# Performance work log

Measured on AMD Instinct MI355X. Metric: run time of the kernel, lower is better.

Reference implementation:

```python
import jax, jax.numpy as jnp
import numpy as np

# Hyper-params from init_kwargs
H, DM, DA, DP, M, T = 8, 512, 256, 128, 32, 4096
DK, DAh, DPh = DM // H, DA // H, DP // H   # 64, 32, 16
B, K_STEPS = 8, 2048
S = T + K_STEPS          # length of x = memory + x_pre
EPS = 1e-12

def _l2n(x):
    # F.normalize(p=2, dim=-1)
    return x / jnp.maximum(jnp.linalg.norm(x, axis=-1, keepdims=True), EPS)

def setup_inputs() -> dict:
    key = jax.random.key(0)
    ks = jax.random.split(key, 28)
    n = lambda i, s, sc=0.05: jax.random.normal(ks[i], s, jnp.float32) * sc
    return {
        "memory": jax.random.normal(ks[0], (B, S - 1, DM), jnp.float32),
        "x_pre":  jax.random.normal(ks[1], (B, 1, DM), jnp.float32),
        "aux":    jax.random.normal(ks[2], (B, S, DA), jnp.float32),
        "pos":    jax.random.normal(ks[3], (B, S, DP), jnp.float32),
        "Wq": n(4, (H, DK, DM)), "bq": n(5, (H, DK)),
        "Wk": n(6, (H, DK, DM)), "bk": n(7, (H, DK)),
        "Wv": n(8, (H, DK, DM)), "bv": n(9, (H, DK)),
        "Wqa": n(10, (H, DAh, DA)), "bqa": n(11, (H, DAh)),
        "Wka": n(12, (H, DAh, DA)), "bka": n(13, (H, DAh)),
        "Wqp": n(14, (H, DPh, DP)), "bqp": n(15, (H, DPh)),
        "Wkp": n(16, (H, DPh, DP)), "bkp": n(17, (H, DPh)),
        "W_ih": n(18, (3 * DK, DM)), "W_hh": n(19, (3 * DK, DK)),
        "b_ih": n(20, (3 * DK,)), "b_hh": n(21, (3 * DK,)),
        "WO": n(22, (DM, DM)), "bO": n(23, (DM,)),
        "w": n(24, (1, 1), 1.0), "w_a": n(25, (1, 1), 1.0), "w_p": n(26, (1, 1), 1.0),
        "G": (jax.random.uniform(ks[27], (DK, DK)) < 0.5).astype(jnp.int32),
        "k": K_STEPS,
    }

def _forward(memory, x_pre, aux, pos, Wq, bq, Wk, bk, Wv, bv, Wqa, bqa, Wka, bka,
             Wqp, bqp, Wkp, bkp, W_ih, W_hh, b_ih, b_hh, WO, bO, w, w_a, w_p, G, k):
    b = memory.shape[0]
    x = jnp.concatenate([memory, x_pre], axis=1)           # [B, S, DM]
    s = x.shape[1]
    Wn = k + T - M + 1                                     # attention window length
    g = G.astype(x.dtype)
    mask_h = jnp.tile(g, (1, H))[None]                     # [1, DK, DM] per-head SparseLinear mask

    # per-head Q/K node projections (SparseLinear), L2-normalized
    Q = _l2n(jnp.einsum('bsd,hkd->bhsk', x, Wq * mask_h) + bq[None, :, None, :])
    K = _l2n(jnp.einsum('bsd,hkd->bhsk', x, Wk * mask_h) + bk[None, :, None, :])

    # tn_transform_pre: for each position p, mean over the M-step window of Qv[m].K[p+m]
    Qv = Q[:, :, -M:, :]                                   # [B,H,M,DK]
    D = jnp.einsum('bhmd,bhsd->bhms', Qv, K)               # [B,H,M,S]
    p_idx = jnp.arange(Wn)[None, :] + jnp.arange(M)[:, None]   # [M,Wn]
    band = D[:, :, jnp.arange(M)[:, None], p_idx]          # [B,H,M,Wn] band-diagonal gather
    tn = band.mean(axis=2)                                 # [B,H,Wn]

    # aux / pos similarities: only the last query row survives the slice in the source
    QA = _l2n(jnp.einsum('bsa,hca->bhsc', aux, Wqa) + bqa[None, :, None, :])
    KA = _l2n(jnp.einsum('bsa,hca->bhsc', aux, Wka) + bka[None, :, None, :])
    dot2 = jnp.einsum('bhc,bhsc->bhs', QA[:, :, -1, :], KA[:, :, aux.shape[1] - Wn:, :])
    QP = _l2n(jnp.einsum('bsp,hcp->bhsc', pos, Wqp) + bqp[None, :, None, :])
    KP = _l2n(jnp.einsum('bsp,hcp->bhsc', pos, Wkp) + bkp[None, :, None, :])
    dot3 = jnp.einsum('bhc,bhsc->bhs', QP[:, :, -1, :], KP[:, :, pos.shape[1] - Wn:, :])

    attn = jax.nn.softmax(w[0, 0] * tn + w_a[0, 0] * dot2 + w_p[0, 0] * dot3, axis=-1)  # [B,H,Wn]

    # value projection over the history window, weighted by attn[..., :-1]
    xv = x[:, s - Wn:s - 1, :]                             # [B, Wn-1, DM]
    V = jnp.einsum('bsd,hkd->bhsk', xv, Wv * mask_h) + bv[None, :, None, :]
    hist = jnp.einsum('bhw,bhwd->bhd', attn[:, :, :-1], V) # [B,H,DK]

    # sequential GRU over the recent M-1 steps (shared across heads)
    recent = jnp.swapaxes(x[:, -M:-1, :], 0, 1)            # [M-1, B, DM]
    def cell(hprev, xt):
        gi = xt @ W_ih.T + b_ih
        gh = hprev @ W_hh.T + b_hh
        ir, iz, inn = jnp.split(gi, 3, axis=-1)
        hr, hz, hn = jnp.split(gh, 3, axis=-1)
        r = jax.nn.sigmoid(ir + hr)
        z = jax.nn.sigmoid(iz + hz)
        nst = jnp.tanh(inn + r * hn)
        return (1.0 - z) * nst + z * hprev, None
    res, _ = jax.lax.scan(cell, jnp.zeros((b, DK), x.dtype), recent)  # [B, DK]

    # concat per-head deltas (deta[:, :, 1:] just drops the initial zeros column)
    deta = (hist + attn[:, :, -1:] * res[:, None, :]).reshape(b, H * DK)   # [B, DM]
    mask_o = jnp.tile(g, (H, H))                           # [DM, DM] for W_O
    out = x_pre + (deta @ (WO * mask_o).T + bO)[:, None, :]
    return out

def reference(memory, x_pre, aux, pos, Wq, bq, Wk, bk, Wv, bv, Wqa, bqa, Wka, bka,
              Wqp, bqp, Wkp, bkp, W_ih, W_hh, b_ih, b_hh, WO, bO, w, w_a, w_p, G, k):
    return _forward(memory, x_pre, aux, pos, Wq, bq, Wk, bk, Wv, bv, Wqa, bqa, Wka,
                    bka, Wqp, bqp, Wkp, bkp, W_ih, W_hh, b_ih, b_hh, WO, bO,
                    w, w_a, w_p, G, k)
```

## Files before the change

### kernel.cpp

```cpp
#include <hip/hip_runtime.h>
#include <math.h>

#define BB   8
#define S    6144
#define SM1  6143
#define DM   512
#define H    8
#define DK   64
#define M    32
#define WN   6113
#define DA   256
#define DAh  32
#define DP   128
#define DPh  16
#define EPSN 1e-12f

#define WS_WKT    0
#define WS_WKAT   262144
#define WS_WKPT   327680
#define WS_QHAT   344064
#define WS_QAHAT  475136
#define WS_QPHAT  477184
#define WS_LOGITS 478208
#define WS_XBAR   869440
#define WS_ALAST  902208
#define WS_RES    902272
#define WS_GI     902784
#define WS_WQM    950400
#define WS_XBF    1212544
#define N_LOGITS  391232
#define N_XBAR    32768

typedef __attribute__((ext_vector_type(8))) short short8;
typedef __attribute__((ext_vector_type(4))) float f32x4;

__device__ inline unsigned short f2bf(float f) {
    union { float f; unsigned u; } v; v.f = f;
    unsigned r = v.u + 0x7fffu + ((v.u >> 16) & 1u);
    return (unsigned short)(r >> 16);
}
__device__ inline float bf2f(unsigned short u) {
    union { unsigned u; float f; } v; v.u = ((unsigned)u) << 16; return v.f;
}

union S8U { short8 v; unsigned short e[8]; };

#define PREP_NB  2368
#define GI_NB    248
#define QAQP_NB  64
#define XCAST_NB 12288

__global__ __launch_bounds__(256) void prelude_k(
    const float* __restrict__ Wk, const float* __restrict__ Wka,
    const float* __restrict__ Wkp, const float* __restrict__ Wq,
    const int* __restrict__ G,
    unsigned short* __restrict__ wkb, unsigned short* __restrict__ wkab,
    unsigned short* __restrict__ wkpb, float* __restrict__ wqm,
    const float* __restrict__ memory, const float* __restrict__ x_pre,
    const float* __restrict__ W_ih, const float* __restrict__ b_ih,
    float* __restrict__ gi_all, unsigned short* __restrict__ xbf,
    const float* __restrict__ aux, const float* __restrict__ pos,
    const float* __restrict__ Wqa, const float* __restrict__ bqa,
    const float* __restrict__ Wqp, const float* __restrict__ bqp,
    float* __restrict__ qahat, float* __restrict__ qphat)
{
    int bx = blockIdx.x, tid = threadIdx.x;
    __shared__ float pa[32][8];
    __shared__ float pp[16][16];

    if (bx < PREP_NB) {
        int idx = bx * 256 + tid;
        if (idx < H*DM*DK) {
            int k = idx & 63; int d = (idx >> 6) & 511; int h = idx >> 15;
            float v = Wk[(size_t)(h*DK + k)*DM + d] * (float)G[k*DK + (d & 63)];
            wkb[(size_t)h*DM*DK + (((d >> 3)*DK + k) << 3) + (d & 7)] = f2bf(v);
        }
        int i2 = idx - H*DM*DK;
        if (i2 >= 0 && i2 < H*DA*DAh) {
            int h = i2 >> 13; int r = i2 & 8191;
            int j = r & 7; int f = r >> 3;
            int c = f & 31; int a = (f >> 5)*8 + j;
            wkab[i2] = f2bf(Wka[(size_t)(h*DAh + c)*DA + a]);
        }
        int i3 = idx - H*DM*DK - H*DA*DAh;
        if (i3 >= 0 && i3 < H*DP*DPh) {
            int h = i3 >> 11; int r = i3 & 2047;
            int j = r & 7; int f = r >> 3;
            int c = f & 15; int p = (f >> 4)*8 + j;
            wkpb[i3] = f2bf(Wkp[(size_t)(h*DPh + c)*DP + p]);
        }
        int i4 = idx - H*DM*DK - H*DA*DAh - H*DP*DPh;
        if (i4 >= 0 && i4 < H*DK*DM) {
            int d = i4 & 511; int k = (i4 >> 9) & 63;
            wqm[i4] = Wq[i4] * (float)G[k*DK + (d & 63)];
        }
        return;
    }
    if (bx < PREP_NB + GI_NB) {
        if (tid < 192) {
            int gx = bx - PREP_NB;
            int t = gx >> 3, b = gx & 7, c = tid;
            const float* xr = memory + ((size_t)b*SM1 + (S - M) + t)*DM;
            const float* wr = W_ih + (size_t)c*DM;
            float s = b_ih[c];
            for (int d = 0; d < DM; d += 4) {
                float4 x4 = *(const float4*)(xr + d);
                float4 w4 = *(const float4*)(wr + d);
                s += x4.x*w4.x + x4.y*w4.y + x4.z*w4.z + x4.w*w4.w;
            }
            gi_all[((size_t)t*BB + b)*192 + c] = s;
        }
        return;
    }
    if (bx < PREP_NB + GI_NB + QAQP_NB) {
        int bh = bx - PREP_NB - GI_NB;
        int b = bh >> 3, h = bh & 7;
        {
            int c = tid & 31, ch = tid >> 5;
            const float* ar = aux + ((size_t)b*S + (S-1))*DA + ch*32;
            const float* wv = Wqa + (size_t)(h*DAh + c)*DA + ch*32;
            float s = 0.f;
            #pragma unroll
            for (int a = 0; a < 32; a += 4) {
                float4 a4 = *(const float4*)(ar + a);
                float4 w4 = *(const float4*)(wv + a);
                s += a4.x*w4.x + a4.y*w4.y + a4.z*w4.z + a4.w*w4.w;
            }
            pa[c][ch] = s;
        }
        {
            int c = tid & 15, ch = tid >> 4;
            const float* pr = pos + ((size_t)b*S + (S-1))*DP + ch*8;
            const float* wv = Wqp + (size_t)(h*DPh + c)*DP + ch*8;
            float4 a4 = *(const float4*)(pr);
            float4 w4 = *(const float4*)(wv);
            float4 a5 = *(const float4*)(pr + 4);
            float4 w5 = *(const float4*)(wv + 4);
            pp[c][ch] = a4.x*w4.x + a4.y*w4.y + a4.z*w4.z + a4.w*w4.w
                      + a5.x*w5.x + a5.y*w5.y + a5.z*w5.z + a5.w*w5.w;
        }
        __syncthreads();
        if (tid < 32) {
            float q = bqa[h*DAh + tid];
            #pragma unroll
            for (int ch = 0; ch < 8; ++ch) q += pa[tid][ch];
            float ss = q*q;
            #pragma unroll
            for (int d2 = 1; d2 <= 16; d2 <<= 1) ss += __shfl_xor(ss, d2);
            qahat[(size_t)bh*DAh + tid] = q / fmaxf(sqrtf(ss), EPSN);
        } else if (tid >= 64 && tid < 80) {
            int c = tid - 64;
            float q = bqp[h*DPh + c];
            #pragma unroll
            for (int ch = 0; ch < 16; ++ch) q += pp[c][ch];
            float ss = q*q;
            #pragma unroll
            for (int d2 = 1; d2 <= 8; d2 <<= 1) ss += __shfl_xor(ss, d2);
            qphat[(size_t)bh*DPh + c] = q / fmaxf(sqrtf(ss), EPSN);
        }
        return;
    }
    {
        size_t e = ((size_t)(bx - PREP_NB - GI_NB - QAQP_NB)*256 + tid)*8;
        int b = (int)(e / ((size_t)S*DM));
        size_t r = e - (size_t)b*S*DM;
        int t = (int)(r >> 9);
        int d = (int)(r & 511);
        const float* src = (t < SM1) ? memory + ((size_t)b*SM1 + t)*DM + d
                                     : x_pre + (size_t)b*DM + d;
        float4 v0 = *(const float4*)src, v1 = *(const float4*)(src + 4);
        S8U t8;
        t8.e[0]=f2bf(v0.x); t8.e[1]=f2bf(v0.y); t8.e[2]=f2bf(v0.z); t8.e[3]=f2bf(v0.w);
        t8.e[4]=f2bf(v1.x); t8.e[5]=f2bf(v1.y); t8.e[6]=f2bf(v1.z); t8.e[7]=f2bf(v1.w);
        *(short8*)(xbf + e) = t8.v;
    }
}

__global__ __launch_bounds__(256) void qhat_gru_k(
    const float* __restrict__ memory, const float* __restrict__ x_pre,
    const float* __restrict__ wqm, const float* __restrict__ bq,
    float* __restrict__ qhat,
    const float* __restrict__ gi_all, const float* __restrict__ W_hh,
    const float* __restrict__ b_hh, float* __restrict__ res)
{
    int bx = blockIdx.x;
    int tid = threadIdx.x;
    __shared__ float part[2][4][64];

    if (bx < 1024) {
        int mp = bx & 15;
        int h  = (bx >> 4) & 7;
        int b  = bx >> 7;
        int k = tid & 63, dq = tid >> 6;

        int m0 = mp*2;
        int t0 = S - M + m0, t1 = t0 + 1;
        const float* x0 = ((t0 < SM1) ? memory + ((size_t)b*SM1 + t0)*DM
                                      : x_pre + (size_t)b*DM) + dq*128;
        const float* x1 = ((t1 < SM1) ? memory + ((size_t)b*SM1 + t1)*DM
                                      : x_pre + (size_t)b*DM) + dq*128;
        const float* wr = wqm + (size_t)(h*DK + k)*DM + dq*128;

        float s0 = 0.f, s1 = 0.f;
        #pragma unroll 8
        for (int d = 0; d < 128; d += 4) {
            float4 w4 = *(const float4*)(wr + d);
            float4 a4 = *(const float4*)(x0 + d);
            float4 b4 = *(const float4*)(x1 + d);
            s0 += w4.x*a4.x + w4.y*a4.y + w4.z*a4.z + w4.w*a4.w;
            s1 += w4.x*b4.x + w4.y*b4.y + w4.z*b4.z + w4.w*b4.w;
        }

        part[0][dq][k] = s0;
        part[1][dq][k] = s1;
        __syncthreads();

        if (tid < 128) {
            int mi = tid >> 6;
            int kk = tid & 63;
            float q = part[mi][0][kk] + part[mi][1][kk] + part[mi][2][kk] + part[mi][3][kk]
                    + bq[h*DK + kk];
            float ss = q*q;
            #pragma unroll
            for (int d2 = 1; d2 <= 32; d2 <<= 1) ss += __shfl_xor(ss, d2);
            qhat[((size_t)(b*H + h)*M + (m0 + mi))*DK + kk] = q / fmaxf(sqrtf(ss), EPSN);
        }
        return;
    }

    {
        int bg = bx - 1024;
        int b = bg*4 + (tid >> 6);
        int l = tid & 63;

        float w0[64], w1[64], w2[64];
        {
            const float* r0p = W_hh + (size_t)l*DK;
            const float* r1p = W_hh + (size_t)(64 + l)*DK;
            const float* r2p = W_hh + (size_t)(128 + l)*DK;
            #pragma unroll
            for (int i = 0; i < 16; ++i) {
                float4 a = *(const float4*)(r0p + i*4);
                w0[i*4]=a.x; w0[i*4+1]=a.y; w0[i*4+2]=a.z; w0[i*4+3]=a.w;
                float4 c = *(const float4*)(r1p + i*4);
                w1[i*4]=c.x; w1[i*4+1]=c.y; w1[i*4+2]=c.z; w1[i*4+3]=c.w;
                float4 e = *(const float4*)(r2p + i*4);
                w2[i*4]=e.x; w2[i*4+1]=e.y; w2[i*4+2]=e.z; w2[i*4+3]=e.w;
            }
        }
        float bh0 = b_hh[l], bh1 = b_hh[64 + l], bh2 = b_hh[128 + l];

        float h = 0.f;
        const float* g0 = gi_all + (size_t)b*192;
        float gr = g0[l], gz = g0[64 + l], gn = g0[128 + l];

        #pragma unroll 1
        for (int t = 0; t < 31; ++t) {
            float a0 = bh0, a1 = bh1, a2 = bh2;
            #pragma unroll
            for (int k = 0; k < 64; ++k) {
                float hk = __int_as_float(__builtin_amdgcn_readlane(__float_as_int(h), k));
                a0 += hk * w0[k];
                a1 += hk * w1[k];
                a2 += hk * w2[k];
            }
            float ngr = 0.f, ngz = 0.f, ngn = 0.f;
            if (t < 30) {
                const float* g2 = gi_all + ((size_t)(t+1)*BB + b)*192;
                ngr = g2[l]; ngz = g2[64 + l]; ngn = g2[128 + l];
            }
            float r = 1.f / (1.f + expf(-(gr + a0)));
            float z = 1.f / (1.f + expf(-(gz + a1)));
            float n = tanhf(gn + r * a2);
            h = (1.f - z)*n + z*h;
            gr = ngr; gz = ngz; gn = ngn;
        }
        res[b*DK + l] = h;
    }
}

#define SMEM_BYTES 16640

__device__ __forceinline__ void kproj3_body(int bxx, int tid, unsigned char* smemraw,
    const unsigned short* __restrict__ xbf, const unsigned short* __restrict__ wkb,
    const float* __restrict__ bk, const float* __restrict__ qhat,
    const float* __restrict__ wscal, float* __restrict__ logits)
{
    int tile = bxx % 96, h = (bxx / 96) & 7, b = bxx / (96*8);
    int t0 = tile * 64;
    int wave = tid >> 6, lane = tid & 63;
    int quad = lane >> 4, l16 = lane & 15;

    typedef unsigned short row72[72];
    row72* Qs = (row72*)smemraw;
    row72* Kb = (row72*)(smemraw + 32*72*2);
    float* tnloc = (float*)(smemraw + 96*72*2);

    {
        const float* qsrc = qhat + (size_t)(b*H + h)*M*DK;
        int i = tid * 8;
        float4 a0 = *(const float4*)(qsrc + i);
        float4 a1 = *(const float4*)(qsrc + i + 4);
        S8U t8;
        t8.e[0]=f2bf(a0.x); t8.e[1]=f2bf(a0.y); t8.e[2]=f2bf(a0.z); t8.e[3]=f2bf(a0.w);
        t8.e[4]=f2bf(a1.x); t8.e[5]=f2bf(a1.y); t8.e[6]=f2bf(a1.z); t8.e[7]=f2bf(a1.w);
        *(short8*)&Qs[i >> 6][i & 63] = t8.v;
    }
    if (tid < 95) tnloc[tid] = 0.f;

    f32x4 acc[4];
    #pragma unroll
    for (int nt = 0; nt < 4; ++nt) acc[nt] = (f32x4){0.f,0.f,0.f,0.f};

    const unsigned short* xrow = xbf + ((size_t)b*S + t0 + wave*16 + l16)*DM;
    const unsigned short* wh = wkb + (size_t)h*DM*DK;

    #pragma unroll
    for (int ch = 0; ch < 4; ++ch) {
        #pragma unroll
        for (int ks = 0; ks < 4; ++ks) {
            short8 a = *(const short8*)(xrow + ch*128 + ks*32 + quad*8);
            #pragma unroll
            for (int nt = 0; nt < 4; ++nt) {
                short8 bf = *(const short8*)(wh + (((ch*16 + ks*4 + quad)*DK) + nt*16 + l16)*8);
                acc[nt] = __builtin_amdgcn_mfma_f32_16x16x32_bf16(a, bf, acc[nt], 0, 0, 0);
            }
        }
    }

    {
        float vv[4][4];
        float ss[4] = {0.f, 0.f, 0.f, 0.f};
        #pragma unroll
        for (int nt = 0; nt < 4; ++nt) {
            float bkv = bk[h*DK + nt*16 + l16];
            #pragma unroll
            for (int reg = 0; reg < 4; ++reg) {
                float v = acc[nt][reg] + bkv;
                vv[nt][reg] = v;
                ss[reg] += v*v;
            }
        }
        #pragma unroll
        for (int d2 = 1; d2 <= 8; d2 <<= 1)
            #pragma unroll
            for (int reg = 0; reg < 4; ++reg) ss[reg] += __shfl_xor(ss[reg], d2);
        #pragma unroll
        for (int reg = 0; reg < 4; ++reg) {
            float inv = 1.f / fmaxf(sqrtf(ss[reg]), EPSN);
            #pragma unroll
            for (int nt = 0; nt < 4; ++nt)
                Kb[wave*16 + quad*4 + reg][nt*16 + l16] = f2bf(vv[nt][reg] * inv);
        }
    }
    __syncthreads();

    {
        int mtile = wave & 1;
        int thalf = (wave >> 1) * 32;
        f32x4 acc2[2];
        acc2[0] = (f32x4){0.f,0.f,0.f,0.f};
        acc2[1] = (f32x4){0.f,0.f,0.f,0.f};
        #pragma unroll
        for (int ks = 0; ks < 2; ++ks) {
            short8 a = *(const short8*)&Qs[mtile*16 + l16][ks*32 + quad*8];
            #pragma unroll
            for (int nt = 0; nt < 2; ++nt) {
                short8 kf = *(const short8*)&Kb[thalf + nt*16 + l16][ks*32 + quad*8];
                acc2[nt] = __builtin_amdgcn_mfma_f32_16x16x32_bf16(a, kf, acc2[nt], 0, 0, 0);
            }
        }
        int m0 = mtile*16 + quad*4;
        #pragma unroll
        for (int nt = 0; nt < 2; ++nt) {
            int tl = thalf + nt*16 + l16;
            #pragma unroll
            for (int reg = 0; reg < 4; ++reg) {
                int mm = m0 + reg;
                int j = t0 + tl - mm;
                if (j >= 0 && j < WN)
                    atomicAdd(&tnloc[tl - mm + 31], acc2[nt][reg]);
            }
        }
    }
    __syncthreads();
    if (tid < 95) {
        int j = t0 + tid - 31;
        if (j >= 0 && j < WN)
            atomicAdd(&logits[(size_t)(b*H + h)*WN + j], wscal[0]*(1.f/32.f)*tnloc[tid]);
    }
}

__device__ __forceinline__ void ka_body(int g, int tid, unsigned char* smemraw,
    const float* __restrict__ aux, const unsigned short* __restrict__ wkab,
    const float* __restrict__ bka, const float* __restrict__ qahat,
    const float* __restrict__ wa, float* __restrict__ logits)
{
    int tile = g % 96;
    int hp   = (g / 96) & 3;
    int b    = g / 384;
    int j0   = tile * 64;
    int wave = tid >> 6, lane = tid & 63;
    int quad = lane >> 4, l16 = lane & 15;

    unsigned short* Xa = (unsigned short*)smemraw;

    int r = tid >> 2, seg = tid & 3;
    int jcl = j0 + r; if (jcl > WN-1) jcl = WN-1;
    int tt = r >> 4, lo = r & 15;
    const float* arb = aux + ((size_t)b*S + (31 + jcl))*DA;

    f32x4 acc[2][2];
    #pragma unroll
    for (int hi = 0; hi < 2; ++hi)
        #pragma unroll
        for (int nt = 0; nt < 2; ++nt) acc[hi][nt] = (f32x4){0.f,0.f,0.f,0.f};

    #pragma unroll
    for (int p = 0; p < 2; ++p) {
        if (p) __syncthreads();
        {
            const float* ar = arb + p*128 + seg*32;
            #pragma unroll
            for (int gg = 0; gg < 4; ++gg) {
                float4 v0 = *(const float4*)(ar + gg*8);
                float4 v1 = *(const float4*)(ar + gg*8 + 4);
                S8U t8;
                t8.e[0]=f2bf(v0.x); t8.e[1]=f2bf(v0.y); t8.e[2]=f2bf(v0.z); t8.e[3]=f2bf(v0.w);
                t8.e[4]=f2bf(v1.x); t8.e[5]=f2bf(v1.y); t8.e[6]=f2bf(v1.z); t8.e[7]=f2bf(v1.w);
                *(short8*)&Xa[(tt*4 + seg)*520 + (gg*16 + lo)*8] = t8.v;
            }
        }
        __syncthreads();
        #pragma unroll
        for (int hi = 0; hi < 2; ++hi) {
            int h = hp*2 + hi;
            const unsigned short* wsrc = wkab + (size_t)h*DA*DAh;
            #pragma unroll
            for (int ks = 0; ks < 4; ++ks) {
                short8 a = *(const short8*)&Xa[(wave*4 + ks)*520 + lane*8];
                #pragma unroll
                for (int nt = 0; nt < 2; ++nt) {
                    short8 bf = *(const short8*)(wsrc +
                        (size_t)((((p*4 + ks)*4 + quad)*32) + nt*16 + l16)*8);
                    acc[hi][nt] = __builtin_amdgcn_mfma_f32_16x16x32_bf16(
                        a, bf, acc[hi][nt], 0, 0, 0);
                }
            }
        }
    }

    float wav = wa[0];
    #pragma unroll
    for (int hi = 0; hi < 2; ++hi) {
        int h = hp*2 + hi;
        float bk0 = bka[h*DAh + l16], bk1 = bka[h*DAh + 16 + l16];
        float q0 = qahat[(size_t)(b*H + h)*DAh + l16];
        float q1 = qahat[(size_t)(b*H + h)*DAh + 16 + l16];
        #pragma unroll
        for (int reg = 0; reg < 4; ++reg) {
            float v0 = acc[hi][0][reg] + bk0;
            float v1 = acc[hi][1][reg] + bk1;
            float ss = v0*v0 + v1*v1;
            float dp = v0*q0 + v1*q1;
            #pragma unroll
            for (int d2 = 1; d2 <= 8; d2 <<= 1) {
                ss += __shfl_xor(ss, d2);
                dp += __shfl_xor(dp, d2);
            }
            if (l16 == 0) {
                int j = j0 + wave*16 + quad*4 + reg;
                if (j < WN)
                    atomicAdd(&logits[(size_t)(b*H + h)*WN + j],
                              wav * dp / fmaxf(sqrtf(ss), EPSN));
            }
        }
    }
}

__device__ __forceinline__ void kp_body(int g, int tid, unsigned char* smemraw,
    const float* __restrict__ pos, const unsigned short* __restrict__ wkpb,
    const float* __restrict__ bkp, const float* __restrict__ qphat,
    const float* __restrict__ wp, float* __restrict__ logits)
{
    int tile = g % 96;
    int hp   = (g / 96) & 3;
    int b    = g / 384;
    int j0   = tile * 64;
    int wave = tid >> 6, lane = tid & 63;
    int quad = lane >> 4, l16 = lane & 15;

    unsigned short* Xp = (unsigned short*)smemraw;

    {
        int r = tid >> 2, seg = tid & 3;
        int j = j0 + r; if (j > WN-1) j = WN-1;
        const float* pr = pos + ((size_t)b*S + (31 + j))*DP + seg*32;
        int tt = r >> 4, lo = r & 15;
        #pragma unroll
        for (int gg = 0; gg < 4; ++gg) {
            float4 v0 = *(const float4*)(pr + gg*8);
            float4 v1 = *(const float4*)(pr + gg*8 + 4);
            int d0 = seg*32 + gg*8;
            int ks = d0 >> 5, qd = (d0 >> 3) & 3;
            S8U t8;
            t8.e[0]=f2bf(v0.x); t8.e[1]=f2bf(v0.y); t8.e[2]=f2bf(v0.z); t8.e[3]=f2bf(v0.w);
            t8.e[4]=f2bf(v1.x); t8.e[5]=f2bf(v1.y); t8.e[6]=f2bf(v1.z); t8.e[7]=f2bf(v1.w);
            *(short8*)&Xp[(tt*4 + ks)*520 + (qd*16 + lo)*8] = t8.v;
        }
    }
    __syncthreads();

    float wpv = wp[0];
    #pragma unroll
    for (int hi = 0; hi < 2; ++hi) {
        int h = hp*2 + hi;
        const unsigned short* wsrc = wkpb + (size_t)h*DP*DPh;
        f32x4 acc = (f32x4){0.f,0.f,0.f,0.f};
        #pragma unroll
        for (int ks = 0; ks < 4; ++ks) {
            short8 a = *(const short8*)&Xp[(wave*4 + ks)*520 + lane*8];
            short8 bf = *(const short8*)(wsrc + (size_t)(((ks*4 + quad)*16) + l16)*8);
            acc = __builtin_amdgcn_mfma_f32_16x16x32_bf16(a, bf, acc, 0, 0, 0);
        }
        float bk0 = bkp[h*DPh + l16];
        float q0 = qphat[(size_t)(b*H + h)*DPh + l16];
        #pragma unroll
        for (int reg = 0; reg < 4; ++reg) {
            float v = acc[reg] + bk0;
            float ss = v*v;
            float dp = v*q0;
            #pragma unroll
            for (int d2 = 1; d2 <= 8; d2 <<= 1) {
                ss += __shfl_xor(ss, d2);
                dp += __shfl_xor(dp, d2);
            }
            if (l16 == 0) {
                int j = j0 + wave*16 + quad*4 + reg;
                if (j < WN)
                    atomicAdd(&logits[(size_t)(b*H + h)*WN + j],
                              wpv * dp / fmaxf(sqrtf(ss), EPSN));
            }
        }
    }
}

#define KA_NB 3072
__global__ __launch_bounds__(256, 4) void proj_fused_k(
    const unsigned short* __restrict__ xbf, const unsigned short* __restrict__ wkb,
    const float* __restrict__ bk, const float* __restrict__ qhat,
    const float* __restrict__ w,
    const float* __restrict__ aux, const unsigned short* __restrict__ wkab,
    const float* __restrict__ bka, const float* __restrict__ qahat,
    const float* __restrict__ wa,
    const float* __restrict__ pos, const unsigned short* __restrict__ wkpb,
    const float* __restrict__ bkp, const float* __restrict__ qphat,
    const float* __restrict__ wp,
    float* __restrict__ logits)
{
    __shared__ __align__(16) unsigned char smemraw[SMEM_BYTES];
    int bx = blockIdx.x;
    int g = bx >> 2, r = bx & 3;
    int tid = threadIdx.x;
    if (r < 2)
        kproj3_body(g*2 + r, tid, smemraw, xbf, wkb, bk, qhat, w, logits);
    else if (r == 2)
        ka_body(g, tid, smemraw, aux, wkab, bka, qahat, wa, logits);
    else
        kp_body(g, tid, smemraw, pos, wkpb, bkp, qphat, wp, logits);
}

__global__ __launch_bounds__(256, 2) void ka_only_k(
    const float* __restrict__ aux, const unsigned short* __restrict__ wkab,
    const float* __restrict__ bka, const float* __restrict__ qahat,
    const float* __restrict__ wa, float* __restrict__ logits)
{
    __shared__ __align__(16) unsigned char smemraw[SMEM_BYTES];
    ka_body(blockIdx.x, threadIdx.x, smemraw, aux, wkab, bka, qahat, wa, logits);
}
__global__ __launch_bounds__(256, 2) void kp_only_k(
    const float* __restrict__ pos, const unsigned short* __restrict__ wkpb,
    const float* __restrict__ bkp, const float* __restrict__ qphat,
    const float* __restrict__ wp, float* __restrict__ logits)
{
    __shared__ __align__(16) unsigned char smemraw[SMEM_BYTES];
    kp_body(blockIdx.x, threadIdx.x, smemraw, pos, wkpb, bkp, qphat, wp, logits);
}

__global__ __launch_bounds__(256, 2) void kproj_band_mfma2(
    const float* __restrict__ memory, const float* __restrict__ x_pre,
    const unsigned short* __restrict__ wkb, const float* __restrict__ bk,
    const float* __restrict__ qhat, const float* __restrict__ wscal,
    float* __restrict__ logits)
{
    int bx = blockIdx.x;
    int hp = bx & 3, b = (bx >> 2) & 7, tile = bx >> 5;
    int t0 = tile * 128;
    int tid = threadIdx.x;
    int wave = tid >> 6, lane = tid & 63;
    int quad = lane >> 4, l16 = lane & 15;

    __shared__ unsigned short Xf[32*520];
    __shared__ unsigned short Wf[16*520];
    __shared__ unsigned short Kb[128][72];
    __shared__ unsigned short Qs[M][72];
    __shared__ float tnloc[159];

    if (tid < 159) tnloc[tid] = 0.f;
    {
        int h = hp*2;
        const float* qsrc = qhat + (size_t)(b*H + h)*M*DK;
        int i = tid * 8;
        float4 a0 = *(const float4*)(qsrc + i);
        float4 a1 = *(const float4*)(qsrc + i + 4);
        S8U t8;
        t8.e[0]=f2bf(a0.x); t8.e[1]=f2bf(a0.y); t8.e[2]=f2bf(a0.z); t8.e[3]=f2bf(a0.w);
        t8.e[4]=f2bf(a1.x); t8.e[5]=f2bf(a1.y); t8.e[6]=f2bf(a1.z); t8.e[7]=f2bf(a1.w);
        *(short8*)&Qs[i >> 6][i & 63] = t8.v;
    }

    f32x4 acc[2][2][4];
    #pragma unroll
    for (int hi = 0; hi < 2; ++hi)
        #pragma unroll
        for (int mt = 0; mt < 2; ++mt)
            #pragma unroll
            for (int nt = 0; nt < 4; ++nt) acc[hi][mt][nt] = (f32x4){0.f,0.f,0.f,0.f};

    for (int ch = 0; ch < 4; ++ch) {
        __syncthreads();
        {
            int r = tid >> 1, half = tid & 1;
            int t = t0 + r;
            const float* xr = ((t < SM1) ? (memory + ((size_t)b*SM1 + t)*DM)
                                         : (x_pre + (size_t)b*DM)) + ch*128 + half*64;
            int tt = r >> 4, lo = r & 15;
            #pragma unroll
            for (int g = 0; g < 8; ++g) {
                float4 v0 = *(const float4*)(xr + g*8);
                float4 v1 = *(const float4*)(xr + g*8 + 4);
                int d0 = half*64 + g*8;
                int ks = d0 >> 5, qd = (d0 >> 3) & 3;
                S8U t8;
                t8.e[0]=f2bf(v0.x); t8.e[1]=f2bf(v0.y); t8.e[2]=f2bf(v0.z); t8.e[3]=f2bf(v0.w);
                t8.e[4]=f2bf(v1.x); t8.e[5]=f2bf(v1.y); t8.e[6]=f2bf(v1.z); t8.e[7]=f2bf(v1.w);
                *(short8*)&Xf[(tt*4 + ks)*520 + (qd*16 + lo)*8] = t8.v;
            }
        }
        {
            const unsigned short* src = wkb + (size_t)(hp*2)*DM*DK + (size_t)ch*8192;
            #pragma unroll
            for (int i = 0; i < 4; ++i) {
                int f = tid + 256*i;
                *(short8*)&Wf[(f >> 6)*520 + (f & 63)*8] = *(const short8*)(src + f*8);
            }
        }
        __syncthreads();
        #pragma unroll
        for (int ks = 0; ks < 4; ++ks) {
            short8 a0 = *(const short8*)&Xf[((wave*2 + 0)*4 + ks)*520 + lane*8];
            short8 a1 = *(const short8*)&Xf[((wave*2 + 1)*4 + ks)*520 + lane*8];
            #pragma unroll
            for (int nt = 0; nt < 4; ++nt) {
                short8 bf = *(const short8*)&Wf[(ks*4 + quad)*520 + (nt*16 + l16)*8];
                acc[0][0][nt] = __builtin_amdgcn_mfma_f32_16x16x32_bf16(a0, bf, acc[0][0][nt], 0, 0, 0);
                acc[0][1][nt] = __builtin_amdgcn_mfma_f32_16x16x32_bf16(a1, bf, acc[0][1][nt], 0, 0, 0);
            }
        }
        __syncthreads();
        {
            const unsigned short* src = wkb + (size_t)(hp*2 + 1)*DM*DK + (size_t)ch*8192;
            #pragma unroll
            for (int i = 0; i < 4; ++i) {
                int f = tid + 256*i;
                *(short8*)&Wf[(f >> 6)*520 + (f & 63)*8] = *(const short8*)(src + f*8);
            }
        }
        __syncthreads();
        #pragma unroll
        for (int ks = 0; ks < 4; ++ks) {
            short8 a0 = *(const short8*)&Xf[((wave*2 + 0)*4 + ks)*520 + lane*8];
            short8 a1 = *(const short8*)&Xf[((wave*2 + 1)*4 + ks)*520 + lane*8];
            #pragma unroll
            for (int nt = 0; nt < 4; ++nt) {
                short8 bf = *(const short8*)&Wf[(ks*4 + quad)*520 + (nt*16 + l16)*8];
                acc[1][0][nt] = __builtin_amdgcn_mfma_f32_16x16x32_bf16(a0, bf, acc[1][0][nt], 0, 0, 0);
                acc[1][1][nt] = __builtin_amdgcn_mfma_f32_16x16x32_bf16(a1, bf, acc[1][1][nt], 0, 0, 0);
            }
        }
    }

    float wom = wscal[0] * (1.f/32.f);

    for (int hi = 0; hi < 2; ++hi) {
        int h = hp*2 + hi;
        __syncthreads();
        {
            float ss[2][4];
            float vv[2][4][4];
            #pragma unroll
            for (int mt = 0; mt < 2; ++mt)
                #pragma unroll
                for (int reg = 0; reg < 4; ++reg) ss[mt][reg] = 0.f;
            #pragma unroll
            for (int nt = 0; nt < 4; ++nt) {
                float bkv = bk[h*DK + nt*16 + l16];
                #pragma unroll
                for (int mt = 0; mt < 2; ++mt)
                    #pragma unroll
                    for (int reg = 0; reg < 4; ++reg) {
                        float v = acc[hi][mt][nt][reg] + bkv;
                        vv[mt][nt][reg] = v;
                        ss[mt][reg] += v*v;
                    }
            }
            #pragma unroll
            for (int d2 = 1; d2 <= 8; d2 <<= 1)
                #pragma unroll
                for (int mt = 0; mt < 2; ++mt)
                    #pragma unroll
                    for (int reg = 0; reg < 4; ++reg)
                        ss[mt][reg] += __shfl_xor(ss[mt][reg], d2);
            #pragma unroll
            for (int mt = 0; mt < 2; ++mt) {
                float inv[4];
                #pragma unroll
                for (int reg = 0; reg < 4; ++reg)
                    inv[reg] = 1.f / fmaxf(sqrtf(ss[mt][reg]), EPSN);
                #pragma unroll
                for (int nt = 0; nt < 4; ++nt)
                    #pragma unroll
                    for (int reg = 0; reg < 4; ++reg)
                        Kb[wave*32 + mt*16 + quad*4 + reg][nt*16 + l16] =
                            f2bf(vv[mt][nt][reg] * inv[reg]);
            }
        }
        __syncthreads();
        {
            f32x4 acc2[2][2];
            #pragma unroll
            for (int mt = 0; mt < 2; ++mt)
                #pragma unroll
                for (int nt = 0; nt < 2; ++nt) acc2[mt][nt] = (f32x4){0.f,0.f,0.f,0.f};
            #pragma unroll
            for (int ks = 0; ks < 2; ++ks) {
                short8 qa0 = *(const short8*)&Qs[l16     ][ks*32 + quad*8];
                short8 qa1 = *(const short8*)&Qs[16 + l16][ks*32 + quad*8];
                #pragma unroll
                for (int nt = 0; nt < 2; ++nt) {
                    short8 kf = *(const short8*)&Kb[wave*32 + nt*16 + l16][ks*32 + quad*8];
                    acc2[0][nt] = __builtin_amdgcn_mfma_f32_16x16x32_bf16(qa0, kf, acc2[0][nt], 0, 0, 0);
                    acc2[1][nt] = __builtin_amdgcn_mfma_f32_16x16x32_bf16(qa1, kf, acc2[1][nt], 0, 0, 0);
                }
            }
            #pragma unroll
            for (int mt = 0; mt < 2; ++mt)
                #pragma unroll
                for (int nt = 0; nt < 2; ++nt) {
                    int tcol = wave*32 + nt*16 + l16;
                    #pragma unroll
                    for (int reg = 0; reg < 4; ++reg) {
                        int m = mt*16 + quad*4 + reg;
                        int j = t0 + tcol - m;
                        if (j >= 0 && j < WN)
                            atomicAdd(&tnloc[tcol - m + 31], acc2[mt][nt][reg]);
                    }
                }
        }
        __syncthreads();
        if (tid < 159) {
            int j = t0 + tid - 31;
            if (j >= 0 && j < WN)
                atomicAdd(&logits[(size_t)(b*H + h)*WN + j], wom * tnloc[tid]);
            tnloc[tid] = 0.f;
        }
        if (hi == 0) {
            const float* qsrc = qhat + (size_t)(b*H + h + 1)*M*DK;
            int i = tid * 8;
            float4 a0 = *(const float4*)(qsrc + i);
            float4 a1 = *(const float4*)(qsrc + i + 4);
            S8U t8;
            t8.e[0]=f2bf(a0.x); t8.e[1]=f2bf(a0.y); t8.e[2]=f2bf(a0.z); t8.e[3]=f2bf(a0.w);
            t8.e[4]=f2bf(a1.x); t8.e[5]=f2bf(a1.y); t8.e[6]=f2bf(a1.z); t8.e[7]=f2bf(a1.w);
            *(short8*)&Qs[i >> 6][i & 63] = t8.v;
        }
    }
}

__global__ __launch_bounds__(1024) void softmax_k(float* __restrict__ logits,
                                                  float* __restrict__ alast)
{
    int bh = blockIdx.x;
    float* L = logits + (size_t)bh*WN;
    __shared__ float red[1024];
    int tid = threadIdx.x;
    float mx = -1e30f;
    for (int j = tid; j < WN; j += 1024) mx = fmaxf(mx, L[j]);
    red[tid] = mx; __syncthreads();
    for (int s2 = 512; s2 > 0; s2 >>= 1) {
        if (tid < s2) red[tid] = fmaxf(red[tid], red[tid+s2]);
        __syncthreads();
    }
    mx = red[0]; __syncthreads();
    float sm = 0.f;
    for (int j = tid; j < WN; j += 1024) sm += expf(L[j] - mx);
    red[tid] = sm; __syncthreads();
    for (int s2 = 512; s2 > 0; s2 >>= 1) {
        if (tid < s2) red[tid] += red[tid+s2];
        __syncthreads();
    }
    float inv = 1.f / red[0];
    for (int j = tid; j < WN; j += 1024) {
        float a = expf(L[j] - mx) * inv;
        L[j] = a;
        if (j == WN-1) alast[bh] = a;
    }
}

#define JC2 96
__global__ __launch_bounds__(256) void xbar_bf_k(
    const unsigned short* __restrict__ xbf, const float* __restrict__ attn,
    float* __restrict__ xbar)
{
    int chunk = blockIdx.x & 63;
    int b = blockIdx.x >> 6;
    int j0 = chunk * JC2;
    int lim = (WN-1) - j0; if (lim > JC2) lim = JC2; if (lim < 0) lim = 0;
    __shared__ float al[H][JC2];
    int tid = threadIdx.x;
    for (int i = tid; i < H*JC2; i += 256) {
        int hh = i / JC2, jj = i - hh*JC2;
        al[hh][jj] = (jj < lim) ? attn[(size_t)(b*H + hh)*WN + j0 + jj] : 0.f;
    }
    __syncthreads();
    int d0 = tid * 2;
    const unsigned* p = (const unsigned*)(xbf + ((size_t)b*S + 31 + j0)*DM + d0);
    float acc[H][2];
    #pragma unroll
    for (int hh = 0; hh < H; ++hh) { acc[hh][0] = 0.f; acc[hh][1] = 0.f; }
    #pragma unroll 4
    for (int jj = 0; jj < lim; ++jj) {
        unsigned u = p[(size_t)jj*(DM/2)];
        float x0 = bf2f((unsigned short)(u & 0xffff));
        float x1 = bf2f((unsigned short)(u >> 16));
        #pragma unroll
        for (int hh = 0; hh < H; ++hh) {
            float a = al[hh][jj];
            acc[hh][0] += a * x0;
            acc[hh][1] += a * x1;
        }
    }
    #pragma unroll
    for (int hh = 0; hh < H; ++hh) {
        atomicAdd(&xbar[(size_t)(b*H+hh)*DM + d0],     acc[hh][0]);
        atomicAdd(&xbar[(size_t)(b*H+hh)*DM + d0 + 1], acc[hh][1]);
    }
}

#define JC 191
__global__ __launch_bounds__(256) void xbar_k(
    const float* __restrict__ memory, const float* __restrict__ attn,
    float* __restrict__ xbar)
{
    int chunk = blockIdx.x & 31;
    int b = blockIdx.x >> 5;
    int j0 = chunk * JC;
    __shared__ float al[H][JC];
    int tid = threadIdx.x;
    for (int i = tid; i < H*JC; i += 256) {
        int hh = i / JC, jj = i - hh*JC;
        al[hh][jj] = attn[(size_t)(b*H + hh)*WN + j0 + jj];
    }
    __syncthreads();
    int d0 = tid * 2;
    float acc[H][2];
    #pragma unroll
    for (int hh = 0; hh < H; ++hh) { acc[hh][0] = 0.f; acc[hh][1] = 0.f; }
    for (int jj = 0; jj < JC; ++jj) {
        int t = 31 + j0 + jj;
        const float2 xv = *(const float2*)(memory + ((size_t)b*SM1 + t)*DM + d0);
        #pragma unroll
        for (int hh = 0; hh < H; ++hh) {
            float a = al[hh][jj];
            acc[hh][0] += a * xv.x;
            acc[hh][1] += a * xv.y;
        }
    }
    #pragma unroll
    for (int hh = 0; hh < H; ++hh) {
        atomicAdd(&xbar[(size_t)(b*H+hh)*DM + d0],     acc[hh][0]);
        atomicAdd(&xbar[(size_t)(b*H+hh)*DM + d0 + 1], acc[hh][1]);
    }
}

__global__ __launch_bounds__(512) void final_k(
    const float* __restrict__ x_pre, const float* __restrict__ xbar,
    const float* __restrict__ Wv, const float* __restrict__ bv,
    const float* __restrict__ WO, const float* __restrict__ bO,
    const float* __restrict__ alast, const float* __restrict__ res,
    const int* __restrict__ G, float* __restrict__ out)
{
    int b = blockIdx.x;
    int tid = threadIdx.x;
    __shared__ float gl[64*64];
    __shared__ float deta[512];
    for (int i = tid; i < 4096; i += 512) gl[i] = (float)G[(i & 63)*64 + (i >> 6)];
    __syncthreads();
    int h = tid >> 6, dk = tid & 63;
    float ala = alast[b*H + h];
    const float* xb  = xbar + (size_t)(b*H + h)*DM;
    const float* wvr = Wv + (size_t)tid*DM;
    const float* gcol = gl + dk;
    float s = 0.f;
    for (int e = 0; e < DM; e += 4) {
        float4 wv4 = *(const float4*)(wvr + e);
        float4 xb4 = *(const float4*)(xb + e);
        int eb = e & 63;
        s += wv4.x*gcol[eb*64]     *xb4.x + wv4.y*gcol[(eb+1)*64]*xb4.y
           + wv4.z*gcol[(eb+2)*64]*xb4.z + wv4.w*gcol[(eb+3)*64]*xb4.w;
    }
    float hist = s + bv[tid]*(1.f - ala);
    deta[tid] = hist + ala * res[b*DK + dk];
    __syncthreads();
    int dpos = tid;
    const float* wor = WO + (size_t)dpos*DM;
    const float* gcol2 = gl + (dpos & 63);
    float o = 0.f;
    for (int jj = 0; jj < DM; jj += 4) {
        float4 wo4 = *(const float4*)(wor + jj);
        int jb = jj & 63;
        o += wo4.x*gcol2[jb*64]     *deta[jj]   + wo4.y*gcol2[(jb+1)*64]*deta[jj+1]
           + wo4.z*gcol2[(jb+2)*64]*deta[jj+2] + wo4.w*gcol2[(jb+3)*64]*deta[jj+3];
    }
    out[(size_t)b*DM + dpos] = x_pre[(size_t)b*DM + dpos] + o + bO[dpos];
}

extern "C" void kernel_launch(void* const* d_in, const int* in_sizes, int n_in,
                              void* d_out, int out_size, void* d_ws, size_t ws_size,
                              hipStream_t stream)
{
    const float* memory = (const float*)d_in[0];
    const float* x_pre  = (const float*)d_in[1];
    const float* aux    = (const float*)d_in[2];
    const float* pos    = (const float*)d_in[3];
    const float* Wq  = (const float*)d_in[4];
    const float* bq  = (const float*)d_in[5];
    const float* Wk  = (const float*)d_in[6];
    const float* bk  = (const float*)d_in[7];
    const float* Wv  = (const float*)d_in[8];
    const float* bv  = (const float*)d_in[9];
    const float* Wqa = (const float*)d_in[10];
    const float* bqa = (const float*)d_in[11];
    const float* Wka = (const float*)d_in[12];
    const float* bka = (const float*)d_in[13];
    const float* Wqp = (const float*)d_in[14];
    const float* bqp = (const float*)d_in[15];
    const float* Wkp = (const float*)d_in[16];
    const float* bkp = (const float*)d_in[17];
    const float* W_ih = (const float*)d_in[18];
    const float* W_hh = (const float*)d_in[19];
    const float* b_ih = (const float*)d_in[20];
    const float* b_hh = (const float*)d_in[21];
    const float* WO  = (const float*)d_in[22];
    const float* bO  = (const float*)d_in[23];
    const float* w   = (const float*)d_in[24];
    const float* w_a = (const float*)d_in[25];
    const float* w_p = (const float*)d_in[26];
    const int*   G   = (const int*)d_in[27];
    (void)in_sizes; (void)n_in; (void)out_size;

    float* ws = (float*)d_ws;
    unsigned short* wkb  = (unsigned short*)(ws + WS_WKT);
    unsigned short* wkab = (unsigned short*)(ws + WS_WKAT);
    unsigned short* wkpb = (unsigned short*)(ws + WS_WKPT);
    float* qhat   = ws + WS_QHAT;
    float* qahat  = ws + WS_QAHAT;
    float* qphat  = ws + WS_QPHAT;
    float* logits = ws + WS_LOGITS;
    float* xbar   = ws + WS_XBAR;
    float* alast  = ws + WS_ALAST;
    float* resb   = ws + WS_RES;
    float* gi_all = ws + WS_GI;
    float* wqm    = ws + WS_WQM;
    unsigned short* xbf = (unsigned short*)(ws + WS_XBF);
    float* outp   = (float*)d_out;

    const size_t need = ((size_t)WS_XBF + 12582912) * 4;
    const bool big = (ws_size >= need);

    hipMemsetAsync(logits, 0, (size_t)(N_LOGITS + N_XBAR)*sizeof(float), stream);

    prelude_k<<<big ? (PREP_NB + GI_NB + QAQP_NB + XCAST_NB)
                    : (PREP_NB + GI_NB + QAQP_NB), 256, 0, stream>>>(
        Wk, Wka, Wkp, Wq, G, wkb, wkab, wkpb, wqm,
        memory, x_pre, W_ih, b_ih, gi_all, xbf,
        aux, pos, Wqa, bqa, Wqp, bqp, qahat, qphat);

    qhat_gru_k<<<1026, 256, 0, stream>>>(memory, x_pre, wqm, bq, qhat,
                                         gi_all, W_hh, b_hh, resb);

    if (big) {
        proj_fused_k<<<12288, 256, 0, stream>>>(
            xbf, wkb, bk, qhat, w,
            aux, wkab, bka, qahat, w_a,
            pos, wkpb, bkp, qphat, w_p, logits);
    } else {
        kproj_band_mfma2<<<48*BB*4, 256, 0, stream>>>(memory, x_pre, wkb, bk, qhat,
                                                      w, logits);
        ka_only_k<<<KA_NB, 256, 0, stream>>>(aux, wkab, bka, qahat, w_a, logits);
        kp_only_k<<<KA_NB, 256, 0, stream>>>(pos, wkpb, bkp, qphat, w_p, logits);
    }

    softmax_k<<<BB*H, 1024, 0, stream>>>(logits, alast);

    if (big)
        xbar_bf_k<<<BB*64, 256, 0, stream>>>(xbf, logits, xbar);
    else
        xbar_k<<<BB*32, 256, 0, stream>>>(memory, logits, xbar);

    final_k<<<BB, 512, 0, stream>>>(x_pre, xbar, Wv, bv, WO, bO, alast, resb, G, outp);
}
```

Measured before the change: 607.1 us.

## Process more heads per block in fused projection kernel to reuse input tiles

The key-projection body now computes two heads per block, reusing each loaded bf16 x fragment for both heads' MFMAs. The aux and pos bodies now handle four heads per block instead of two, so each staged input tile serves more heads. The fused grid is halved to match. This cuts redundant global reads of x, aux and pos and the bf16 conversion work, in exchange for more accumulator registers and fewer blocks, which may reduce occupancy or latency hiding.

```diff
diff --git a/kernel.cpp b/kernel.cpp
--- a/kernel.cpp
+++ b/kernel.cpp
@@ -279,115 +279,132 @@
     }
 }
 
-#define SMEM_BYTES 16640
-
-__device__ __forceinline__ void kproj3_body(int bxx, int tid, unsigned char* smemraw,
+#define SMEM_BYTES 18816
+
+__device__ __forceinline__ void kproj2h_body(int bxx, int tid, unsigned char* smemraw,
     const unsigned short* __restrict__ xbf, const unsigned short* __restrict__ wkb,
     const float* __restrict__ bk, const float* __restrict__ qhat,
     const float* __restrict__ wscal, float* __restrict__ logits)
 {
-    int tile = bxx % 96, h = (bxx / 96) & 7, b = bxx / (96*8);
+    int tile = bxx % 96, hp = (bxx / 96) & 3, b = bxx / 384;
+    int h0 = hp*2;
     int t0 = tile * 64;
     int wave = tid >> 6, lane = tid & 63;
     int quad = lane >> 4, l16 = lane & 15;
 
     typedef unsigned short row72[72];
     row72* Qs = (row72*)smemraw;
-    row72* Kb = (row72*)(smemraw + 32*72*2);
-    float* tnloc = (float*)(smemraw + 96*72*2);
+    row72* Kb = (row72*)(smemraw + 64*72*2);
+    float* tnloc = (float*)(smemraw + 128*72*2);
 
     {
-        const float* qsrc = qhat + (size_t)(b*H + h)*M*DK;
         int i = tid * 8;
-        float4 a0 = *(const float4*)(qsrc + i);
-        float4 a1 = *(const float4*)(qsrc + i + 4);
-        S8U t8;
-        t8.e[0]=f2bf(a0.x); t8.e[1]=f2bf(a0.y); t8.e[2]=f2bf(a0.z); t8.e[3]=f2bf(a0.w);
-        t8.e[4]=f2bf(a1.x); t8.e[5]=f2bf(a1.y); t8.e[6]=f2bf(a1.z); t8.e[7]=f2bf(a1.w);
-        *(short8*)&Qs[i >> 6][i & 63] = t8.v;
+        #pragma unroll
+        for (int hi = 0; hi < 2; ++hi) {
+            const float* qsrc = qhat + (size_t)(b*H + h0 + hi)*M*DK;
+            float4 a0 = *(const float4*)(qsrc + i);
+            float4 a1 = *(const float4*)(qsrc + i + 4);
+            S8U t8;
+            t8.e[0]=f2bf(a0.x); t8.e[1]=f2bf(a0.y); t8.e[2]=f2bf(a0.z); t8.e[3]=f2bf(a0.w);
+            t8.e[4]=f2bf(a1.x); t8.e[5]=f2bf(a1.y); t8.e[6]=f2bf(a1.z); t8.e[7]=f2bf(a1.w);
+            *(short8*)&Qs[hi*32 + (i >> 6)][i & 63] = t8.v;
+        }
     }
     if (tid < 95) tnloc[tid] = 0.f;
 
-    f32x4 acc[4];
-    #pragma unroll
-    for (int nt = 0; nt < 4; ++nt) acc[nt] = (f32x4){0.f,0.f,0.f,0.f};
+    f32x4 acc[2][4];
+    #pragma unroll
+    for (int hi = 0; hi < 2; ++hi)
+        #pragma unroll
+        for (int nt = 0; nt < 4; ++nt) acc[hi][nt] = (f32x4){0.f,0.f,0.f,0.f};
 
     const unsigned short* xrow = xbf + ((size_t)b*S + t0 + wave*16 + l16)*DM;
-    const unsigned short* wh = wkb + (size_t)h*DM*DK;
+    const unsigned short* wh0 = wkb + (size_t)h0*DM*DK;
+    const unsigned short* wh1 = wh0 + (size_t)DM*DK;
 
     #pragma unroll
     for (int ch = 0; ch < 4; ++ch) {
         #pragma unroll
         for (int ks = 0; ks < 4; ++ks) {
             short8 a = *(const short8*)(xrow + ch*128 + ks*32 + quad*8);
+            size_t boff = (size_t)(((ch*16 + ks*4 + quad)*DK))*8;
             #pragma unroll
             for (int nt = 0; nt < 4; ++nt) {
-                short8 bf = *(const short8*)(wh + (((ch*16 + ks*4 + quad)*DK) + nt*16 + l16)*8);
-                acc[nt] = __builtin_amdgcn_mfma_f32_16x16x32_bf16(a, bf, acc[nt], 0, 0, 0);
-            }
-        }
-    }
-
-    {
-        float vv[4][4];
-        float ss[4] = {0.f, 0.f, 0.f, 0.f};
-        #pragma unroll
-        for (int nt = 0; nt < 4; ++nt) {
-            float bkv = bk[h*DK + nt*16 + l16];
+                short8 bf0 = *(const short8*)(wh0 + boff + (nt*16 + l16)*8);
+                short8 bf1 = *(const short8*)(wh1 + boff + (nt*16 + l16)*8);
+                acc[0][nt] = __builtin_amdgcn_mfma_f32_16x16x32_bf16(a, bf0, acc[0][nt], 0, 0, 0);
+                acc[1][nt] = __builtin_amdgcn_mfma_f32_16x16x32_bf16(a, bf1, acc[1][nt], 0, 0, 0);
+            }
+        }
+    }
+
+    float wom = wscal[0] * (1.f/32.f);
+
+    #pragma unroll
+    for (int hi = 0; hi < 2; ++hi) {
+        int h = h0 + hi;
+        __syncthreads();
+        {
+            float vv[4][4];
+            float ss[4] = {0.f, 0.f, 0.f, 0.f};
+            #pragma unroll
+            for (int nt = 0; nt < 4; ++nt) {
+                float bkv = bk[h*DK + nt*16 + l16];
+                #pragma unroll
+                for (int reg = 0; reg < 4; ++reg) {
+                    float v = acc[hi][nt][reg] + bkv;
+                    vv[nt][reg] = v;
+                    ss[reg] += v*v;
+                }
+            }
+            #pragma unroll
+            for (int d2 = 1; d2 <= 8; d2 <<= 1)
+                #pragma unroll
+                for (int reg = 0; reg < 4; ++reg) ss[reg] += __shfl_xor(ss[reg], d2);
             #pragma unroll
             for (int reg = 0; reg < 4; ++reg) {
-                float v = acc[nt][reg] + bkv;
-                vv[nt][reg] = v;
-                ss[reg] += v*v;
-            }
-        }
-        #pragma unroll
-        for (int d2 = 1; d2 <= 8; d2 <<= 1)
-            #pragma unroll
-            for (int reg = 0; reg < 4; ++reg) ss[reg] += __shfl_xor(ss[reg], d2);
-        #pragma unroll
-        for (int reg = 0; reg < 4; ++reg) {
-            float inv = 1.f / fmaxf(sqrtf(ss[reg]), EPSN);
-            #pragma unroll
-            for (int nt = 0; nt < 4; ++nt)
-                Kb[wave*16 + quad*4 + reg][nt*16 + l16] = f2bf(vv[nt][reg] * inv);
-        }
-    }
-    __syncthreads();
-
-    {
-        int mtile = wave & 1;
-        int thalf = (wave >> 1) * 32;
-        f32x4 acc2[2];
-        acc2[0] = (f32x4){0.f,0.f,0.f,0.f};
-        acc2[1] = (f32x4){0.f,0.f,0.f,0.f};
-        #pragma unroll
-        for (int ks = 0; ks < 2; ++ks) {
-            short8 a = *(const short8*)&Qs[mtile*16 + l16][ks*32 + quad*8];
+                float inv = 1.f / fmaxf(sqrtf(ss[reg]), EPSN);
+                #pragma unroll
+                for (int nt = 0; nt < 4; ++nt)
+                    Kb[wave*16 + quad*4 + reg][nt*16 + l16] = f2bf(vv[nt][reg] * inv);
+            }
+        }
+        __syncthreads();
+        {
+            int mtile = wave & 1;
+            int thalf = (wave >> 1) * 32;
+            f32x4 acc2[2];
+            acc2[0] = (f32x4){0.f,0.f,0.f,0.f};
+            acc2[1] = (f32x4){0.f,0.f,0.f,0.f};
+            #pragma unroll
+            for (int ks = 0; ks < 2; ++ks) {
+                short8 a = *(const short8*)&Qs[hi*32 + mtile*16 + l16][ks*32 + quad*8];
+                #pragma unroll
+                for (int nt = 0; nt < 2; ++nt) {
+                    short8 kf = *(const short8*)&Kb[thalf + nt*16 + l16][ks*32 + quad*8];
+                    acc2[nt] = __builtin_amdgcn_mfma_f32_16x16x32_bf16(a, kf, acc2[nt], 0, 0, 0);
+                }
+            }
+            int m0 = mtile*16 + quad*4;
             #pragma unroll
             for (int nt = 0; nt < 2; ++nt) {
-                short8 kf = *(const short8*)&Kb[thalf + nt*16 + l16][ks*32 + quad*8];
-                acc2[nt] = __builtin_amdgcn_mfma_f32_16x16x32_bf16(a, kf, acc2[nt], 0, 0, 0);
-            }
-        }
-        int m0 = mtile*16 + quad*4;
-        #pragma unroll
-        for (int nt = 0; nt < 2; ++nt) {
-            int tl = thalf + nt*16 + l16;
-            #pragma unroll
-            for (int reg = 0; reg < 4; ++reg) {
-                int mm = m0 + reg;
-                int j = t0 + tl - mm;
-                if (j >= 0 && j < WN)
-                    atomicAdd(&tnloc[tl - mm + 31], acc2[nt][reg]);
-            }
-        }
-    }
-    __syncthreads();
-    if (tid < 95) {
-        int j = t0 + tid - 31;
-        if (j >= 0 && j < WN)
-            atomicAdd(&logits[(size_t)(b*H + h)*WN + j], wscal[0]*(1.f/32.f)*tnloc[tid]);
+                int tl = thalf + nt*16 + l16;
+                #pragma unroll
+                for (int reg = 0; reg < 4; ++reg) {
+                    int mm = m0 + reg;
+                    int j = t0 + tl - mm;
+                    if (j >= 0 && j < WN)
+                        atomicAdd(&tnloc[tl - mm + 31], acc2[nt][reg]);
+                }
+            }
+        }
+        __syncthreads();
+        if (tid < 95) {
+            int j = t0 + tid - 31;
+            if (j >= 0 && j < WN)
+                atomicAdd(&logits[(size_t)(b*H + h)*WN + j], wom * tnloc[tid]);
+            tnloc[tid] = 0.f;
+        }
     }
 }
 
@@ -397,8 +414,8 @@
     const float* __restrict__ wa, float* __restrict__ logits)
 {
     int tile = g % 96;
-    int hp   = (g / 96) & 3;
-    int b    = g / 384;
+    int hp   = (g / 96) & 1;
+    int b    = g / 192;
     int j0   = tile * 64;
     int wave = tid >> 6, lane = tid & 63;
     int quad = lane >> 4, l16 = lane & 15;
@@ -410,9 +427,9 @@
     int tt = r >> 4, lo = r & 15;
     const float* arb = aux + ((size_t)b*S + (31 + jcl))*DA;
 
-    f32x4 acc[2][2];
-    #pragma unroll
-    for (int hi = 0; hi < 2; ++hi)
+    f32x4 acc[4][2];
+    #pragma unroll
+    for (int hi = 0; hi < 4; ++hi)
         #pragma unroll
         for (int nt = 0; nt < 2; ++nt) acc[hi][nt] = (f32x4){0.f,0.f,0.f,0.f};
 
@@ -433,12 +450,12 @@
         }
         __syncthreads();
         #pragma unroll
-        for (int hi = 0; hi < 2; ++hi) {
-            int h = hp*2 + hi;
-            const unsigned short* wsrc = wkab + (size_t)h*DA*DAh;
-            #pragma unroll
-            for (int ks = 0; ks < 4; ++ks) {
-                short8 a = *(const short8*)&Xa[(wave*4 + ks)*520 + lane*8];
+        for (int ks = 0; ks < 4; ++ks) {
+            short8 a = *(const short8*)&Xa[(wave*4 + ks)*520 + lane*8];
+            #pragma unroll
+            for (int hi = 0; hi < 4; ++hi) {
+                int h = hp*4 + hi;
+                const unsigned short* wsrc = wkab + (size_t)h*DA*DAh;
                 #pragma unroll
                 for (int nt = 0; nt < 2; ++nt) {
                     short8 bf = *(const short8*)(wsrc +
@@ -452,8 +469,8 @@
 
     float wav = wa[0];
     #pragma unroll
-    for (int hi = 0; hi < 2; ++hi) {
-        int h = hp*2 + hi;
+    for (int hi = 0; hi < 4; ++hi) {
+        int h = hp*4 + hi;
         float bk0 = bka[h*DAh + l16], bk1 = bka[h*DAh + 16 + l16];
         float q0 = qahat[(size_t)(b*H + h)*DAh + l16];
         float q1 = qahat[(size_t)(b*H + h)*DAh + 16 + l16];
@@ -484,8 +501,8 @@
     const float* __restrict__ wp, float* __restrict__ logits)
 {
     int tile = g % 96;
-    int hp   = (g / 96) & 3;
-    int b    = g / 384;
+    int hp   = (g / 96) & 1;
+    int b    = g / 192;
     int j0   = tile * 64;
     int wave = tid >> 6, lane = tid & 63;
     int quad = lane >> 4, l16 = lane & 15;
@@ -511,23 +528,31 @@
     }
     __syncthreads();
 
+    f32x4 acc[4];
+    #pragma unroll
+    for (int hi = 0; hi < 4; ++hi) acc[hi] = (f32x4){0.f,0.f,0.f,0.f};
+
+    #pragma unroll
+    for (int ks = 0; ks < 4; ++ks) {
+        short8 a = *(const short8*)&Xp[(wave*4 + ks)*520 + lane*8];
+        #pragma unroll
+        for (int hi = 0; hi < 4; ++hi) {
+            int h = hp*4 + hi;
+            const unsigned short* wsrc = wkpb + (size_t)h*DP*DPh;
+            short8 bf = *(const short8*)(wsrc + (size_t)(((ks*4 + quad)*16) + l16)*8);
+            acc[hi] = __builtin_amdgcn_mfma_f32_16x16x32_bf16(a, bf, acc[hi], 0, 0, 0);
+        }
+    }
+
     float wpv = wp[0];
     #pragma unroll
-    for (int hi = 0; hi < 2; ++hi) {
-        int h = hp*2 + hi;
-        const unsigned short* wsrc = wkpb + (size_t)h*DP*DPh;
-        f32x4 acc = (f32x4){0.f,0.f,0.f,0.f};
-        #pragma unroll
-        for (int ks = 0; ks < 4; ++ks) {
-            short8 a = *(const short8*)&Xp[(wave*4 + ks)*520 + lane*8];
-            short8 bf = *(const short8*)(wsrc + (size_t)(((ks*4 + quad)*16) + l16)*8);
-            acc = __builtin_amdgcn_mfma_f32_16x16x32_bf16(a, bf, acc, 0, 0, 0);
-        }
+    for (int hi = 0; hi < 4; ++hi) {
+        int h = hp*4 + hi;
         float bk0 = bkp[h*DPh + l16];
         float q0 = qphat[(size_t)(b*H + h)*DPh + l16];
         #pragma unroll
         for (int reg = 0; reg < 4; ++reg) {
-            float v = acc[reg] + bk0;
+            float v = acc[hi][reg] + bk0;
             float ss = v*v;
             float dp = v*q0;
             #pragma unroll
@@ -545,7 +570,7 @@
     }
 }
 
-#define KA_NB 3072
+#define KA_NB 1536
 __global__ __launch_bounds__(256, 4) void proj_fused_k(
     const unsigned short* __restrict__ xbf, const unsigned short* __restrict__ wkb,
     const float* __restrict__ bk, const float* __restrict__ qhat,
@@ -563,7 +588,7 @@
     int g = bx >> 2, r = bx & 3;
     int tid = threadIdx.x;
     if (r < 2)
-        kproj3_body(g*2 + r, tid, smemraw, xbf, wkb, bk, qhat, w, logits);
+        kproj2h_body(g*2 + r, tid, smemraw, xbf, wkb, bk, qhat, w, logits);
     else if (r == 2)
         ka_body(g, tid, smemraw, aux, wkab, bka, qahat, wa, logits);
     else
@@ -1000,7 +1025,7 @@
                                          gi_all, W_hh, b_hh, resb);
 
     if (big) {
-        proj_fused_k<<<12288, 256, 0, stream>>>(
+        proj_fused_k<<<6144, 256, 0, stream>>>(
             xbf, wkb, bk, qhat, w,
             aux, wkab, bka, qahat, w_a,
             pos, wkpb, bkp, qphat, w_p, logits);
```

New measurement: 584.4 us. 1.04x faster.
